# Kernel tuning notes

Hardware: AMD Instinct MI355X
Metric: run time of the kernel (lower is better)

Reference implementation:

```python
import jax, jax.numpy as jnp
import numpy as np

B, N1, N2, D = 4096, 16, 32, 30   # node batch, 1st-hop nbrs, 2nd-hop nbrs, nodeDataLen
H, HD = 6, 5                       # heads, head_dim (embed_dim = size_out*heads = 30)
LH = 64                            # linear_hidden
NEG_SLOPE = 0.02


def setup_inputs() -> dict:
    key = jax.random.key(0)
    ks = jax.random.split(key, 20)
    def w(k, shape, std=0.2):
        return jax.random.normal(k, shape, dtype=jnp.float32) * std
    return {
        "x2": jax.random.normal(ks[0], (B, N1, N2, D), dtype=jnp.float32),
        "self_feat": jax.random.normal(ks[1], (B, D), dtype=jnp.float32),
        # second-hop GraphLayer params (size_in=30 -> embed 30)
        "lin_w2": w(ks[2], (D, D)), "lin_b2": jnp.zeros((D,), jnp.float32),
        "in_w2": w(ks[3], (3 * D, D), 0.1), "in_b2": jnp.zeros((3 * D,), jnp.float32),
        "out_w2": w(ks[4], (D, D), 0.1), "out_b2": jnp.zeros((D,), jnp.float32),
        # first-hop GraphLayer params
        "lin_w1": w(ks[5], (D, D)), "lin_b1": jnp.zeros((D,), jnp.float32),
        "in_w1": w(ks[6], (3 * D, D), 0.1), "in_b1": jnp.zeros((3 * D,), jnp.float32),
        "out_w1": w(ks[7], (D, D), 0.1), "out_b1": jnp.zeros((D,), jnp.float32),
        # classification MLP
        "cw1": w(ks[8], (LH, D), 0.02), "cb1": jnp.zeros((LH,), jnp.float32),
        "cw2": w(ks[9], (LH, LH), 0.02), "cb2": jnp.zeros((LH,), jnp.float32),
        "cw3": w(ks[10], (2, LH), 0.02), "cb3": jnp.zeros((2,), jnp.float32),
    }


def graph_layer(x, lw, lb, iw, ib, ow, ob):
    """x: [S, D] -> Linear + LeakyReLU(0.02) + MHA(self) + mean over S -> [D].
    Dropout(0.2) is identity in eval mode."""
    S = x.shape[0]
    y = jax.nn.leaky_relu(x @ lw.T + lb, NEG_SLOPE)          # [S, D]
    qkv = y @ iw.T + ib                                       # [S, 3D] packed in_proj
    q, k, v = jnp.split(qkv, 3, axis=-1)
    q = q.reshape(S, H, HD)
    k = k.reshape(S, H, HD)
    v = v.reshape(S, H, HD)
    scores = jnp.einsum('shd,thd->hst', q, k) / np.float32(np.sqrt(HD))
    att = jax.nn.softmax(scores, axis=-1)                     # [H, S, S]
    o = jnp.einsum('hst,thd->shd', att, v).reshape(S, H * HD) # [S, D]
    o = o @ ow.T + ob
    return o.mean(axis=0)                                     # [D]


def reference(x2, self_feat,
              lin_w2, lin_b2, in_w2, in_b2, out_w2, out_b2,
              lin_w1, lin_b1, in_w1, in_b1, out_w1, out_b1,
              cw1, cb1, cw2, cb2, cw3, cb3):
    gl2 = lambda x: graph_layer(x, lin_w2, lin_b2, in_w2, in_b2, out_w2, out_b2)
    h1 = jax.vmap(jax.vmap(gl2))(x2)                          # [B, N1, D] second-hop aggregation
    seq = jnp.concatenate([h1, self_feat[:, None, :]], axis=1)  # [B, N1+1, D] append current node
    gl1 = lambda x: graph_layer(x, lin_w1, lin_b1, in_w1, in_b1, out_w1, out_b1)
    emb = jax.vmap(gl1)(seq)                                  # [B, D]
    h = jax.nn.leaky_relu(emb @ cw1.T + cb1, NEG_SLOPE)
    h = jax.nn.leaky_relu(h @ cw2.T + cb2, NEG_SLOPE)
    logits = h @ cw3.T + cb3                                  # [B, 2]
    # original applies Softmax(dim=0) to the 1-D 2-vector per node == softmax over classes
    return jax.nn.softmax(logits, axis=-1)
```

## Files before the change

kernel.cpp:

```cpp
#include <hip/hip_runtime.h>
#include <math.h>

#define LRELU(v) fmaxf((v), 0.02f * (v))

typedef __attribute__((ext_vector_type(8)))  short short8;
typedef __attribute__((ext_vector_type(4)))  float f32x4;
typedef __attribute__((ext_vector_type(16))) float f32x16;
typedef __attribute__((ext_vector_type(2)))  int   int2v;
typedef __attribute__((ext_vector_type(4)))  int   int4v;

__device__ inline short f2bf(float f) {
    unsigned u = __builtin_bit_cast(unsigned, f);
    unsigned r = (u + 0x7FFFu + ((u >> 16) & 1u)) >> 16;
    return (short)r;
}
__device__ inline int cvt_pk_bf16(float lo, float hi) {
    int r;
    asm("v_cvt_pk_bf16_f32 %0, %1, %2" : "=v"(r) : "v"(lo), "v"(hi));
    return r;
}
__device__ inline float exp2_asm(float x) {
    float r;
    asm("v_exp_f32 %0, %1" : "=v"(r) : "v"(x));
    return r;
}

#define RS5L  0.6451994329f

__global__ __launch_bounds__(256, 4) void fused_kernel(
    const float* __restrict__ x2, const float* __restrict__ self_feat,
    const float* __restrict__ lw2, const float* __restrict__ lb2,
    const float* __restrict__ iw2, const float* __restrict__ ib2,
    const float* __restrict__ ow2, const float* __restrict__ ob2,
    const float* __restrict__ lw1, const float* __restrict__ lb1,
    const float* __restrict__ iw1, const float* __restrict__ ib1,
    const float* __restrict__ ow1, const float* __restrict__ ob1,
    const float* __restrict__ cw1, const float* __restrict__ cb1,
    const float* __restrict__ cw2, const float* __restrict__ cb2,
    const float* __restrict__ cw3, const float* __restrict__ cb3,
    float* __restrict__ out)
{
    __shared__ __attribute__((aligned(16))) short y_lds[2][32][40];
    __shared__ __attribute__((aligned(16))) short qmf[2][6][33][8];
    __shared__ __attribute__((aligned(16))) short kmf[2][6][33][8];
    __shared__ __attribute__((aligned(16))) short vbf[2][6][8][40];
    __shared__ __attribute__((aligned(16))) float h1fp[2][16][33];
    __shared__ float obar1[32];
    __shared__ float embb[32];
    __shared__ float hb1[64];
    __shared__ float hb2[64];
    __shared__ float lg[2];

    const int tid  = threadIdx.x;
    const int lane = tid & 63;
    const int w    = tid >> 6;
    const int l15  = lane & 15;
    const int lq   = lane >> 4;
    const int h5   = lane >> 5;
    const int scol = lane & 31;
    const int rowz = (lane < 32) ? scol : 32;

    for (int i = tid; i < 1584; i += 256) { ((int*)qmf)[i] = 0; ((int*)kmf)[i] = 0; }
    for (int i = tid; i < 1920; i += 256) ((int*)vbf)[i] = 0;
    if (tid < 2) obar1[30 + tid] = 0.0f;

    const int di = w & 1, si = w >> 1;
    const int jtA = (3 * w) >> 1, jtB = (3 * w + 2) >> 1;
    short8 blw2f; float lbv2v;
    {
        int d = di * 16 + l15;
        #pragma unroll
        for (int i = 0; i < 8; ++i) {
            int k = lq * 8 + i;
            blw2f[i] = f2bf((d < 30 && k < 30) ? lw2[d * 30 + k] : 0.0f);
        }
        lbv2v = (d < 30) ? lb2[d] : 0.0f;
    }
    short8 biwA2, biwB2; float ibvA2, ibvB2;
    {
        int jA = jtA * 16 + l15, jB = jtB * 16 + l15;
        #pragma unroll
        for (int i = 0; i < 8; ++i) {
            int k = lq * 8 + i;
            biwA2[i] = f2bf((jA < 90 && k < 30) ? iw2[jA * 30 + k] : 0.0f);
            biwB2[i] = f2bf((jB < 90 && k < 30) ? iw2[jB * 30 + k] : 0.0f);
        }
        ibvA2 = (jA < 90) ? ib2[jA] : 0.0f;
        ibvB2 = (jB < 90) ? ib2[jB] : 0.0f;
    }
    __syncthreads();

    const long node = (long)blockIdx.x;
    const float* xbase = x2 + node * (16L * 960);
    const float* sfp   = self_feat + node * 30;
    const int dd = (scol < 30) ? scol : 0;

    for (int it = 0; it < 8; ++it) {

        {
            int s = si * 16 + l15;
            #pragma unroll
            for (int pr = 0; pr < 2; ++pr) {
                const float* xr = xbase + (2 * it + pr) * 960 + s * 30 + lq * 8;
                float xv[8];
                #pragma unroll
                for (int i = 0; i < 8; ++i) {
                    int k = lq * 8 + i;
                    xv[i] = (k < 30) ? xr[i] : 0.0f;
                }
                int4v ai;
                ai.x = cvt_pk_bf16(xv[0], xv[1]);
                ai.y = cvt_pk_bf16(xv[2], xv[3]);
                ai.z = cvt_pk_bf16(xv[4], xv[5]);
                ai.w = cvt_pk_bf16(xv[6], xv[7]);
                short8 af = __builtin_bit_cast(short8, ai);
                f32x4 c = {0.0f, 0.0f, 0.0f, 0.0f};
                c = __builtin_amdgcn_mfma_f32_16x16x32_bf16(af, blw2f, c, 0, 0, 0);
                float y0 = LRELU(c[0] + lbv2v), y1 = LRELU(c[1] + lbv2v);
                float y2 = LRELU(c[2] + lbv2v), y3 = LRELU(c[3] + lbv2v);
                int p01 = cvt_pk_bf16(y0, y1), p23 = cvt_pk_bf16(y2, y3);
                int row = si * 16 + lq * 4, col = di * 16 + l15;
                y_lds[pr][row + 0][col] = (short)p01;
                y_lds[pr][row + 1][col] = (short)(p01 >> 16);
                y_lds[pr][row + 2][col] = (short)p23;
                y_lds[pr][row + 3][col] = (short)(p23 >> 16);
            }
        }
        __syncthreads();

        {
            #pragma unroll
            for (int pr = 0; pr < 2; ++pr) {
                short8 a0 = *(const short8*)&y_lds[pr][l15][lq * 8];
                short8 a1 = *(const short8*)&y_lds[pr][16 + l15][lq * 8];
                #pragma unroll
                for (int t = 0; t < 3; ++t) {
                    int T = 3 * w + t, jt = T >> 1, si_ = T & 1;
                    short8 a = si_ ? a1 : a0;
                    short8 b = (jt == jtA) ? biwA2 : biwB2;
                    float ibv = (jt == jtA) ? ibvA2 : ibvB2;
                    f32x4 c = {0.0f, 0.0f, 0.0f, 0.0f};
                    c = __builtin_amdgcn_mfma_f32_16x16x32_bf16(a, b, c, 0, 0, 0);
                    int j = jt * 16 + l15;
                    int s0 = si_ * 16 + lq * 4;
                    if (j < 30) {
                        int h = j / 5, e = j - 5 * h;
                        int p01 = cvt_pk_bf16(c[0] + ibv, c[1] + ibv);
                        int p23 = cvt_pk_bf16(c[2] + ibv, c[3] + ibv);
                        qmf[pr][h][s0 + 0][e] = (short)p01;
                        qmf[pr][h][s0 + 1][e] = (short)(p01 >> 16);
                        qmf[pr][h][s0 + 2][e] = (short)p23;
                        qmf[pr][h][s0 + 3][e] = (short)(p23 >> 16);
                    } else if (j < 60) {
                        int jj = j - 30; int h = jj / 5, e = jj - 5 * h;
                        float ibl = ibv * RS5L;
                        int p01 = cvt_pk_bf16(fmaf(c[0], RS5L, ibl), fmaf(c[1], RS5L, ibl));
                        int p23 = cvt_pk_bf16(fmaf(c[2], RS5L, ibl), fmaf(c[3], RS5L, ibl));
                        kmf[pr][h][s0 + 0][e] = (short)p01;
                        kmf[pr][h][s0 + 1][e] = (short)(p01 >> 16);
                        kmf[pr][h][s0 + 2][e] = (short)p23;
                        kmf[pr][h][s0 + 3][e] = (short)(p23 >> 16);
                    } else if (j < 90) {
                        int jj = j - 60; int h = jj / 5, e = jj - 5 * h;
                        int k0 = ((s0 >> 1) & 4) | ((s0 << 1) & 8) | (s0 & 16);
                        int2v wv;
                        wv.x = cvt_pk_bf16(c[0] + ibv, c[1] + ibv);
                        wv.y = cvt_pk_bf16(c[2] + ibv, c[3] + ibv);
                        *(int2v*)&vbf[pr][h][e][k0] = wv;
                    }
                }
            }
        }
        __syncthreads();

        {
            const int pr  = w >> 1;
            const int grp = w & 1;
            float smv0, smv1, smv2;
            #pragma unroll
            for (int hh = 0; hh < 3; ++hh) {
                const int h = 3 * grp + hh;
                short8 af = *(const short8*)&kmf[pr][h][rowz][0];
                short8 bf = *(const short8*)&qmf[pr][h][rowz][0];
                f32x16 c;
                #pragma unroll
                for (int r = 0; r < 16; ++r) c[r] = 0.0f;
                c = __builtin_amdgcn_mfma_f32_32x32x16_bf16(af, bf, c, 0, 0, 0);
                float m = c[0];
                #pragma unroll
                for (int r = 1; r < 16; ++r) m = fmaxf(m, c[r]);
                m = fmaxf(m, __shfl_xor(m, 32));
                float Z = 0.0f;
                #pragma unroll
                for (int r = 0; r < 16; ++r) { c[r] = exp2_asm(c[r] - m); Z += c[r]; }
                Z += __shfl_xor(Z, 32);
                float rZ = __builtin_amdgcn_rcpf(Z) * (1.0f / 32.0f);
                int4v a1i, a2i;
                a1i.x = cvt_pk_bf16(c[0] * rZ,  c[1] * rZ);
                a1i.y = cvt_pk_bf16(c[2] * rZ,  c[3] * rZ);
                a1i.z = cvt_pk_bf16(c[4] * rZ,  c[5] * rZ);
                a1i.w = cvt_pk_bf16(c[6] * rZ,  c[7] * rZ);
                a2i.x = cvt_pk_bf16(c[8] * rZ,  c[9] * rZ);
                a2i.y = cvt_pk_bf16(c[10] * rZ, c[11] * rZ);
                a2i.z = cvt_pk_bf16(c[12] * rZ, c[13] * rZ);
                a2i.w = cvt_pk_bf16(c[14] * rZ, c[15] * rZ);
                short8 b1 = *(const short8*)&vbf[pr][h][scol & 7][8 * h5];
                short8 b2 = *(const short8*)&vbf[pr][h][scol & 7][16 + 8 * h5];
                f32x16 P;
                #pragma unroll
                for (int r = 0; r < 16; ++r) P[r] = 0.0f;
                P = __builtin_amdgcn_mfma_f32_32x32x16_bf16(
                        __builtin_bit_cast(short8, a1i), b1, P, 0, 0, 0);
                P = __builtin_amdgcn_mfma_f32_32x32x16_bf16(
                        __builtin_bit_cast(short8, a2i), b2, P, 0, 0, 0);
                float sm = 0.0f;
                #pragma unroll
                for (int r = 0; r < 16; ++r) sm += P[r];
                sm += __shfl_xor(sm, 32);
                if (hh == 0) smv0 = sm; else if (hh == 1) smv1 = sm; else smv2 = sm;
            }
            float part = 0.0f;
            #pragma unroll
            for (int hh = 0; hh < 3; ++hh) {
                float smv = (hh == 0) ? smv0 : (hh == 1) ? smv1 : smv2;
                #pragma unroll
                for (int e = 0; e < 5; ++e) {
                    float ov = __shfl(smv, e);
                    part = fmaf(ov, ow2[dd * 30 + grp * 15 + hh * 5 + e], part);
                }
            }
            if (lane < 30) h1fp[grp][2 * it + pr][lane] = part;
        }
    }
    __syncthreads();

    short8 blw1f; float lbv1v;
    {
        int d = di * 16 + l15;
        #pragma unroll
        for (int i = 0; i < 8; ++i) {
            int k = lq * 8 + i;
            blw1f[i] = f2bf((d < 30 && k < 30) ? lw1[d * 30 + k] : 0.0f);
        }
        lbv1v = (d < 30) ? lb1[d] : 0.0f;
    }
    short8 biwA1, biwB1; float ibvA1, ibvB1;
    {
        int jA = jtA * 16 + l15, jB = jtB * 16 + l15;
        #pragma unroll
        for (int i = 0; i < 8; ++i) {
            int k = lq * 8 + i;
            biwA1[i] = f2bf((jA < 90 && k < 30) ? iw1[jA * 30 + k] : 0.0f);
            biwB1[i] = f2bf((jB < 90 && k < 30) ? iw1[jB * 30 + k] : 0.0f);
        }
        ibvA1 = (jA < 90) ? ib1[jA] : 0.0f;
        ibvB1 = (jB < 90) ? ib1[jB] : 0.0f;
    }

    {
        float xv[8];
        if (si == 0) {
            #pragma unroll
            for (int i = 0; i < 8; ++i) {
                int k = lq * 8 + i;
                xv[i] = (k < 30)
                    ? (h1fp[0][l15][k] + h1fp[1][l15][k] + ob2[k]) : 0.0f;
            }
        } else {
            #pragma unroll
            for (int i = 0; i < 8; ++i) {
                int k = lq * 8 + i;
                xv[i] = (l15 == 0 && k < 30) ? sfp[k] : 0.0f;
            }
        }
        int4v ai;
        ai.x = cvt_pk_bf16(xv[0], xv[1]);
        ai.y = cvt_pk_bf16(xv[2], xv[3]);
        ai.z = cvt_pk_bf16(xv[4], xv[5]);
        ai.w = cvt_pk_bf16(xv[6], xv[7]);
        short8 af = __builtin_bit_cast(short8, ai);
        f32x4 c = {0.0f, 0.0f, 0.0f, 0.0f};
        c = __builtin_amdgcn_mfma_f32_16x16x32_bf16(af, blw1f, c, 0, 0, 0);
        float y0 = LRELU(c[0] + lbv1v), y1 = LRELU(c[1] + lbv1v);
        float y2 = LRELU(c[2] + lbv1v), y3 = LRELU(c[3] + lbv1v);
        int p01 = cvt_pk_bf16(y0, y1), p23 = cvt_pk_bf16(y2, y3);
        int row = si * 16 + lq * 4, col = di * 16 + l15;
        y_lds[0][row + 0][col] = (short)p01;
        y_lds[0][row + 1][col] = (short)(p01 >> 16);
        y_lds[0][row + 2][col] = (short)p23;
        y_lds[0][row + 3][col] = (short)(p23 >> 16);
    }
    __syncthreads();

    {
        short8 a0 = *(const short8*)&y_lds[0][l15][lq * 8];
        short8 a1 = *(const short8*)&y_lds[0][16 + l15][lq * 8];
        #pragma unroll
        for (int t = 0; t < 3; ++t) {
            int T = 3 * w + t, jt = T >> 1, si_ = T & 1;
            short8 a = si_ ? a1 : a0;
            short8 b = (jt == jtA) ? biwA1 : biwB1;
            float ibv = (jt == jtA) ? ibvA1 : ibvB1;
            f32x4 c = {0.0f, 0.0f, 0.0f, 0.0f};
            c = __builtin_amdgcn_mfma_f32_16x16x32_bf16(a, b, c, 0, 0, 0);
            int j = jt * 16 + l15;
            int s0 = si_ * 16 + lq * 4;
            if (j < 30) {
                int h = j / 5, e = j - 5 * h;
                int p01 = cvt_pk_bf16(c[0] + ibv, c[1] + ibv);
                int p23 = cvt_pk_bf16(c[2] + ibv, c[3] + ibv);
                qmf[0][h][s0 + 0][e] = (short)p01;
                qmf[0][h][s0 + 1][e] = (short)(p01 >> 16);
                qmf[0][h][s0 + 2][e] = (short)p23;
                qmf[0][h][s0 + 3][e] = (short)(p23 >> 16);
            } else if (j < 60) {
                int jj = j - 30; int h = jj / 5, e = jj - 5 * h;
                float ibl = ibv * RS5L;
                int p01 = cvt_pk_bf16(fmaf(c[0], RS5L, ibl), fmaf(c[1], RS5L, ibl));
                int p23 = cvt_pk_bf16(fmaf(c[2], RS5L, ibl), fmaf(c[3], RS5L, ibl));
                kmf[0][h][s0 + 0][e] = (short)p01;
                kmf[0][h][s0 + 1][e] = (short)(p01 >> 16);
                kmf[0][h][s0 + 2][e] = (short)p23;
                kmf[0][h][s0 + 3][e] = (short)(p23 >> 16);
            } else if (j < 90) {
                int jj = j - 60; int h = jj / 5, e = jj - 5 * h;
                int k0 = ((s0 >> 1) & 4) | ((s0 << 1) & 8) | (s0 & 16);
                int2v wv;
                wv.x = cvt_pk_bf16(c[0] + ibv, c[1] + ibv);
                wv.y = cvt_pk_bf16(c[2] + ibv, c[3] + ibv);
                *(int2v*)&vbf[0][h][e][k0] = wv;
            }
        }
    }
    __syncthreads();

    if (w < 3) {
        #pragma unroll
        for (int hh = 0; hh < 2; ++hh) {
            const int h = 2 * w + hh;
            short8 af = *(const short8*)&kmf[0][h][rowz][0];
            short8 bf = *(const short8*)&qmf[0][h][rowz][0];
            f32x16 c;
            #pragma unroll
            for (int r = 0; r < 16; ++r) c[r] = 0.0f;
            c = __builtin_amdgcn_mfma_f32_32x32x16_bf16(af, bf, c, 0, 0, 0);
            #pragma unroll
            for (int r = 0; r < 16; ++r) {
                int tr = (r & 3) + 8 * (r >> 2) + 4 * h5;
                c[r] = (tr < 17) ? c[r] : -1e30f;
            }
            float m = c[0];
            #pragma unroll
            for (int r = 1; r < 16; ++r) m = fmaxf(m, c[r]);
            m = fmaxf(m, __shfl_xor(m, 32));
            float Z = 0.0f;
            #pragma unroll
            for (int r = 0; r < 16; ++r) { c[r] = exp2_asm(c[r] - m); Z += c[r]; }
            Z += __shfl_xor(Z, 32);
            float rZ = __builtin_amdgcn_rcpf(Z) * (1.0f / 17.0f);
            int4v a1i, a2i;
            a1i.x = cvt_pk_bf16(c[0] * rZ,  c[1] * rZ);
            a1i.y = cvt_pk_bf16(c[2] * rZ,  c[3] * rZ);
            a1i.z = cvt_pk_bf16(c[4] * rZ,  c[5] * rZ);
            a1i.w = cvt_pk_bf16(c[6] * rZ,  c[7] * rZ);
            a2i.x = cvt_pk_bf16(c[8] * rZ,  c[9] * rZ);
            a2i.y = cvt_pk_bf16(c[10] * rZ, c[11] * rZ);
            a2i.z = cvt_pk_bf16(c[12] * rZ, c[13] * rZ);
            a2i.w = cvt_pk_bf16(c[14] * rZ, c[15] * rZ);
            short8 b1 = *(const short8*)&vbf[0][h][scol & 7][8 * h5];
            short8 b2 = *(const short8*)&vbf[0][h][scol & 7][16 + 8 * h5];
            f32x16 P;
            #pragma unroll
            for (int r = 0; r < 16; ++r) P[r] = 0.0f;
            P = __builtin_amdgcn_mfma_f32_32x32x16_bf16(
                    __builtin_bit_cast(short8, a1i), b1, P, 0, 0, 0);
            P = __builtin_amdgcn_mfma_f32_32x32x16_bf16(
                    __builtin_bit_cast(short8, a2i), b2, P, 0, 0, 0);
            float sm = 0.0f;
            #pragma unroll
            for (int r = 0; r < 8; ++r) sm += P[r];
            sm += (h5 == 0) ? P[8] : 0.0f;
            sm += __shfl_xor(sm, 32);
            if (lane < 5) obar1[h * 5 + lane] = sm;
        }
    }
    __syncthreads();

    if (tid < 240) {
        const int d = tid >> 3, jq = tid & 7;
        f32x4 ov = *(const f32x4*)&obar1[jq * 4];
        float part = 0.0f;
        #pragma unroll
        for (int i = 0; i < 4; ++i) {
            int j = jq * 4 + i;
            if (j < 30) part = fmaf(ov[i], ow1[d * 30 + j], part);
        }
        part += __shfl_down(part, 4, 8);
        part += __shfl_down(part, 2, 8);
        part += __shfl_down(part, 1, 8);
        if (jq == 0) embb[d] = part + ob1[d];
    }
    __syncthreads();

    {
        const int o = tid >> 2, kq = tid & 3;
        float part = 0.0f;
        #pragma unroll
        for (int i = 0; i < 8; ++i) {
            int k = kq * 8 + i;
            if (k < 30) part = fmaf(embb[k], cw1[o * 30 + k], part);
        }
        part += __shfl_down(part, 2, 4);
        part += __shfl_down(part, 1, 4);
        if (kq == 0) hb1[o] = LRELU(part + cb1[o]);
    }
    __syncthreads();
    {
        const int o = tid >> 2, kq = tid & 3;
        float part = 0.0f;
        #pragma unroll
        for (int i = 0; i < 16; ++i) {
            int k = kq * 16 + i;
            part = fmaf(hb1[k], cw2[o * 64 + k], part);
        }
        part += __shfl_down(part, 2, 4);
        part += __shfl_down(part, 1, 4);
        if (kq == 0) hb2[o] = LRELU(part + cb2[o]);
    }
    __syncthreads();
    if (tid < 128) {
        const int c = tid >> 6, k = tid & 63;
        float part = hb2[k] * cw3[c * 64 + k];
        part += __shfl_down(part, 32);
        part += __shfl_down(part, 16);
        part += __shfl_down(part, 8);
        part += __shfl_down(part, 4);
        part += __shfl_down(part, 2);
        part += __shfl_down(part, 1);
        if (k == 0) lg[c] = part + cb3[c];
    }
    __syncthreads();
    if (tid < 2) {
        float m = fmaxf(lg[0], lg[1]);
        float e0 = __expf(lg[0] - m), e1 = __expf(lg[1] - m);
        float pr = ((tid == 0) ? e0 : e1) / (e0 + e1);
        out[node * 2 + tid] = pr;
    }
}

extern "C" void kernel_launch(void* const* d_in, const int* in_sizes, int n_in,
                              void* d_out, int out_size, void* d_ws, size_t ws_size,
                              hipStream_t stream)
{
    const float* x2        = (const float*)d_in[0];
    const float* self_feat = (const float*)d_in[1];
    const float* lin_w2 = (const float*)d_in[2];
    const float* lin_b2 = (const float*)d_in[3];
    const float* in_w2  = (const float*)d_in[4];
    const float* in_b2  = (const float*)d_in[5];
    const float* out_w2 = (const float*)d_in[6];
    const float* out_b2 = (const float*)d_in[7];
    const float* lin_w1 = (const float*)d_in[8];
    const float* lin_b1 = (const float*)d_in[9];
    const float* in_w1  = (const float*)d_in[10];
    const float* in_b1  = (const float*)d_in[11];
    const float* out_w1 = (const float*)d_in[12];
    const float* out_b1 = (const float*)d_in[13];
    const float* cw1 = (const float*)d_in[14];
    const float* cb1 = (const float*)d_in[15];
    const float* cw2 = (const float*)d_in[16];
    const float* cb2 = (const float*)d_in[17];
    const float* cw3 = (const float*)d_in[18];
    const float* cb3 = (const float*)d_in[19];
    float* outp = (float*)d_out;

    fused_kernel<<<4096, 256, 0, stream>>>(
        x2, self_feat,
        lin_w2, lin_b2, in_w2, in_b2, out_w2, out_b2,
        lin_w1, lin_b1, in_w1, in_b1, out_w1, out_b1,
        cw1, cb1, cw2, cb2, cw3, cb3, outp);
}
```

Before: 497.6 us.

## Process one neighbor per iteration with register prefetch of next x tile

Changes the second-hop loop from two neighbors per iteration (8 iterations) to one neighbor per iteration (16 iterations), halving the LDS buffers. The global loads for the next neighbor are issued into registers before the current neighbor's MFMA work, overlapping memory latency with compute. Attention heads are redistributed across all four waves (2,2,1,1), and partial outputs are kept per wave and summed at the end. Each step now does less work per barrier and has uneven work across waves, but the smaller LDS footprint may allow higher occupancy.

```diff
diff --git a/kernel.cpp b/kernel.cpp
--- a/kernel.cpp
+++ b/kernel.cpp
@@ -40,11 +40,11 @@
     const float* __restrict__ cw3, const float* __restrict__ cb3,
     float* __restrict__ out)
 {
-    __shared__ __attribute__((aligned(16))) short y_lds[2][32][40];
-    __shared__ __attribute__((aligned(16))) short qmf[2][6][33][8];
-    __shared__ __attribute__((aligned(16))) short kmf[2][6][33][8];
-    __shared__ __attribute__((aligned(16))) short vbf[2][6][8][40];
-    __shared__ __attribute__((aligned(16))) float h1fp[2][16][33];
+    __shared__ __attribute__((aligned(16))) short y_lds[32][40];
+    __shared__ __attribute__((aligned(16))) short qmf[6][33][8];
+    __shared__ __attribute__((aligned(16))) short kmf[6][33][8];
+    __shared__ __attribute__((aligned(16))) short vbf[6][8][40];
+    __shared__ __attribute__((aligned(16))) float h1fp[4][16][33];
     __shared__ float obar1[32];
     __shared__ float embb[32];
     __shared__ float hb1[64];
@@ -60,8 +60,8 @@
     const int scol = lane & 31;
     const int rowz = (lane < 32) ? scol : 32;
 
-    for (int i = tid; i < 1584; i += 256) { ((int*)qmf)[i] = 0; ((int*)kmf)[i] = 0; }
-    for (int i = tid; i < 1920; i += 256) ((int*)vbf)[i] = 0;
+    for (int i = tid; i < 792; i += 256) { ((int*)qmf)[i] = 0; ((int*)kmf)[i] = 0; }
+    for (int i = tid; i < 960; i += 256) ((int*)vbf)[i] = 0;
     if (tid < 2) obar1[30 + tid] = 0.0f;
 
     const int di = w & 1, si = w >> 1;
@@ -94,94 +94,100 @@
     const float* xbase = x2 + node * (16L * 960);
     const float* sfp   = self_feat + node * 30;
     const int dd = (scol < 30) ? scol : 0;
-
-    for (int it = 0; it < 8; ++it) {
+    const int srow = si * 16 + l15;
+
+    float xcur[8];
+    {
+        const float* xr = xbase + srow * 30 + lq * 8;
+        #pragma unroll
+        for (int i = 0; i < 8; ++i) {
+            int k = lq * 8 + i;
+            xcur[i] = (k < 30) ? xr[i] : 0.0f;
+        }
+    }
+
+    for (int it = 0; it < 16; ++it) {
+        float xnext[8];
 
         {
-            int s = si * 16 + l15;
-            #pragma unroll
-            for (int pr = 0; pr < 2; ++pr) {
-                const float* xr = xbase + (2 * it + pr) * 960 + s * 30 + lq * 8;
-                float xv[8];
-                #pragma unroll
-                for (int i = 0; i < 8; ++i) {
-                    int k = lq * 8 + i;
-                    xv[i] = (k < 30) ? xr[i] : 0.0f;
+            int4v ai;
+            ai.x = cvt_pk_bf16(xcur[0], xcur[1]);
+            ai.y = cvt_pk_bf16(xcur[2], xcur[3]);
+            ai.z = cvt_pk_bf16(xcur[4], xcur[5]);
+            ai.w = cvt_pk_bf16(xcur[6], xcur[7]);
+            const int itn = (it < 15) ? it + 1 : it;
+            const float* xr = xbase + itn * 960 + srow * 30 + lq * 8;
+            #pragma unroll
+            for (int i = 0; i < 8; ++i) {
+                int k = lq * 8 + i;
+                xnext[i] = (k < 30) ? xr[i] : 0.0f;
+            }
+            short8 af = __builtin_bit_cast(short8, ai);
+            f32x4 c = {0.0f, 0.0f, 0.0f, 0.0f};
+            c = __builtin_amdgcn_mfma_f32_16x16x32_bf16(af, blw2f, c, 0, 0, 0);
+            float y0 = LRELU(c[0] + lbv2v), y1 = LRELU(c[1] + lbv2v);
+            float y2 = LRELU(c[2] + lbv2v), y3 = LRELU(c[3] + lbv2v);
+            int p01 = cvt_pk_bf16(y0, y1), p23 = cvt_pk_bf16(y2, y3);
+            int row = si * 16 + lq * 4, col = di * 16 + l15;
+            y_lds[row + 0][col] = (short)p01;
+            y_lds[row + 1][col] = (short)(p01 >> 16);
+            y_lds[row + 2][col] = (short)p23;
+            y_lds[row + 3][col] = (short)(p23 >> 16);
+        }
+        __syncthreads();
+
+        {
+            short8 a0 = *(const short8*)&y_lds[l15][lq * 8];
+            short8 a1 = *(const short8*)&y_lds[16 + l15][lq * 8];
+            #pragma unroll
+            for (int t = 0; t < 3; ++t) {
+                int T = 3 * w + t, jt = T >> 1, si_ = T & 1;
+                short8 a = si_ ? a1 : a0;
+                short8 b = (jt == jtA) ? biwA2 : biwB2;
+                float ibv = (jt == jtA) ? ibvA2 : ibvB2;
+                f32x4 c = {0.0f, 0.0f, 0.0f, 0.0f};
+                c = __builtin_amdgcn_mfma_f32_16x16x32_bf16(a, b, c, 0, 0, 0);
+                int j = jt * 16 + l15;
+                int s0 = si_ * 16 + lq * 4;
+                if (j < 30) {
+                    int h = j / 5, e = j - 5 * h;
+                    int p01 = cvt_pk_bf16(c[0] + ibv, c[1] + ibv);
+                    int p23 = cvt_pk_bf16(c[2] + ibv, c[3] + ibv);
+                    qmf[h][s0 + 0][e] = (short)p01;
+                    qmf[h][s0 + 1][e] = (short)(p01 >> 16);
+                    qmf[h][s0 + 2][e] = (short)p23;
+                    qmf[h][s0 + 3][e] = (short)(p23 >> 16);
+                } else if (j < 60) {
+                    int jj = j - 30; int h = jj / 5, e = jj - 5 * h;
+                    float ibl = ibv * RS5L;
+                    int p01 = cvt_pk_bf16(fmaf(c[0], RS5L, ibl), fmaf(c[1], RS5L, ibl));
+                    int p23 = cvt_pk_bf16(fmaf(c[2], RS5L, ibl), fmaf(c[3], RS5L, ibl));
+                    kmf[h][s0 + 0][e] = (short)p01;
+                    kmf[h][s0 + 1][e] = (short)(p01 >> 16);
+                    kmf[h][s0 + 2][e] = (short)p23;
+                    kmf[h][s0 + 3][e] = (short)(p23 >> 16);
+                } else if (j < 90) {
+                    int jj = j - 60; int h = jj / 5, e = jj - 5 * h;
+                    int k0 = ((s0 >> 1) & 4) | ((s0 << 1) & 8) | (s0 & 16);
+                    int2v wv;
+                    wv.x = cvt_pk_bf16(c[0] + ibv, c[1] + ibv);
+                    wv.y = cvt_pk_bf16(c[2] + ibv, c[3] + ibv);
+                    *(int2v*)&vbf[h][e][k0] = wv;
                 }
-                int4v ai;
-                ai.x = cvt_pk_bf16(xv[0], xv[1]);
-                ai.y = cvt_pk_bf16(xv[2], xv[3]);
-                ai.z = cvt_pk_bf16(xv[4], xv[5]);
-                ai.w = cvt_pk_bf16(xv[6], xv[7]);
-                short8 af = __builtin_bit_cast(short8, ai);
-                f32x4 c = {0.0f, 0.0f, 0.0f, 0.0f};
-                c = __builtin_amdgcn_mfma_f32_16x16x32_bf16(af, blw2f, c, 0, 0, 0);
-                float y0 = LRELU(c[0] + lbv2v), y1 = LRELU(c[1] + lbv2v);
-                float y2 = LRELU(c[2] + lbv2v), y3 = LRELU(c[3] + lbv2v);
-                int p01 = cvt_pk_bf16(y0, y1), p23 = cvt_pk_bf16(y2, y3);
-                int row = si * 16 + lq * 4, col = di * 16 + l15;
-                y_lds[pr][row + 0][col] = (short)p01;
-                y_lds[pr][row + 1][col] = (short)(p01 >> 16);
-                y_lds[pr][row + 2][col] = (short)p23;
-                y_lds[pr][row + 3][col] = (short)(p23 >> 16);
             }
         }
         __syncthreads();
 
         {
-            #pragma unroll
-            for (int pr = 0; pr < 2; ++pr) {
-                short8 a0 = *(const short8*)&y_lds[pr][l15][lq * 8];
-                short8 a1 = *(const short8*)&y_lds[pr][16 + l15][lq * 8];
-                #pragma unroll
-                for (int t = 0; t < 3; ++t) {
-                    int T = 3 * w + t, jt = T >> 1, si_ = T & 1;
-                    short8 a = si_ ? a1 : a0;
-                    short8 b = (jt == jtA) ? biwA2 : biwB2;
-                    float ibv = (jt == jtA) ? ibvA2 : ibvB2;
-                    f32x4 c = {0.0f, 0.0f, 0.0f, 0.0f};
-                    c = __builtin_amdgcn_mfma_f32_16x16x32_bf16(a, b, c, 0, 0, 0);
-                    int j = jt * 16 + l15;
-                    int s0 = si_ * 16 + lq * 4;
-                    if (j < 30) {
-                        int h = j / 5, e = j - 5 * h;
-                        int p01 = cvt_pk_bf16(c[0] + ibv, c[1] + ibv);
-                        int p23 = cvt_pk_bf16(c[2] + ibv, c[3] + ibv);
-                        qmf[pr][h][s0 + 0][e] = (short)p01;
-                        qmf[pr][h][s0 + 1][e] = (short)(p01 >> 16);
-                        qmf[pr][h][s0 + 2][e] = (short)p23;
-                        qmf[pr][h][s0 + 3][e] = (short)(p23 >> 16);
-                    } else if (j < 60) {
-                        int jj = j - 30; int h = jj / 5, e = jj - 5 * h;
-                        float ibl = ibv * RS5L;
-                        int p01 = cvt_pk_bf16(fmaf(c[0], RS5L, ibl), fmaf(c[1], RS5L, ibl));
-                        int p23 = cvt_pk_bf16(fmaf(c[2], RS5L, ibl), fmaf(c[3], RS5L, ibl));
-                        kmf[pr][h][s0 + 0][e] = (short)p01;
-                        kmf[pr][h][s0 + 1][e] = (short)(p01 >> 16);
-                        kmf[pr][h][s0 + 2][e] = (short)p23;
-                        kmf[pr][h][s0 + 3][e] = (short)(p23 >> 16);
-                    } else if (j < 90) {
-                        int jj = j - 60; int h = jj / 5, e = jj - 5 * h;
-                        int k0 = ((s0 >> 1) & 4) | ((s0 << 1) & 8) | (s0 & 16);
-                        int2v wv;
-                        wv.x = cvt_pk_bf16(c[0] + ibv, c[1] + ibv);
-                        wv.y = cvt_pk_bf16(c[2] + ibv, c[3] + ibv);
-                        *(int2v*)&vbf[pr][h][e][k0] = wv;
-                    }
-                }
-            }
-        }
-        __syncthreads();
-
-        {
-            const int pr  = w >> 1;
-            const int grp = w & 1;
-            float smv0, smv1, smv2;
-            #pragma unroll
-            for (int hh = 0; hh < 3; ++hh) {
-                const int h = 3 * grp + hh;
-                short8 af = *(const short8*)&kmf[pr][h][rowz][0];
-                short8 bf = *(const short8*)&qmf[pr][h][rowz][0];
+            const int hbase = (w < 2) ? (2 * w) : (2 + w);
+            const bool two = (w < 2);
+            float smv0 = 0.0f, smv1 = 0.0f;
+            #pragma unroll
+            for (int hh = 0; hh < 2; ++hh) {
+                if (hh == 1 && !two) continue;
+                const int h = hbase + hh;
+                short8 af = *(const short8*)&kmf[h][rowz][0];
+                short8 bf = *(const short8*)&qmf[h][rowz][0];
                 f32x16 c;
                 #pragma unroll
                 for (int r = 0; r < 16; ++r) c[r] = 0.0f;
@@ -204,8 +210,8 @@
                 a2i.y = cvt_pk_bf16(c[10] * rZ, c[11] * rZ);
                 a2i.z = cvt_pk_bf16(c[12] * rZ, c[13] * rZ);
                 a2i.w = cvt_pk_bf16(c[14] * rZ, c[15] * rZ);
-                short8 b1 = *(const short8*)&vbf[pr][h][scol & 7][8 * h5];
-                short8 b2 = *(const short8*)&vbf[pr][h][scol & 7][16 + 8 * h5];
+                short8 b1 = *(const short8*)&vbf[h][scol & 7][8 * h5];
+                short8 b2 = *(const short8*)&vbf[h][scol & 7][16 + 8 * h5];
                 f32x16 P;
                 #pragma unroll
                 for (int r = 0; r < 16; ++r) P[r] = 0.0f;
@@ -217,20 +223,25 @@
                 #pragma unroll
                 for (int r = 0; r < 16; ++r) sm += P[r];
                 sm += __shfl_xor(sm, 32);
-                if (hh == 0) smv0 = sm; else if (hh == 1) smv1 = sm; else smv2 = sm;
+                if (hh == 0) smv0 = sm; else smv1 = sm;
             }
             float part = 0.0f;
             #pragma unroll
-            for (int hh = 0; hh < 3; ++hh) {
-                float smv = (hh == 0) ? smv0 : (hh == 1) ? smv1 : smv2;
+            for (int e = 0; e < 5; ++e) {
+                float ov = __shfl(smv0, e);
+                part = fmaf(ov, ow2[dd * 30 + hbase * 5 + e], part);
+            }
+            if (two) {
                 #pragma unroll
                 for (int e = 0; e < 5; ++e) {
-                    float ov = __shfl(smv, e);
-                    part = fmaf(ov, ow2[dd * 30 + grp * 15 + hh * 5 + e], part);
+                    float ov = __shfl(smv1, e);
+                    part = fmaf(ov, ow2[dd * 30 + (hbase + 1) * 5 + e], part);
                 }
             }
-            if (lane < 30) h1fp[grp][2 * it + pr][lane] = part;
-        }
+            if (lane < 30) h1fp[w][it][lane] = part;
+        }
+        #pragma unroll
+        for (int i = 0; i < 8; ++i) xcur[i] = xnext[i];
     }
     __syncthreads();
 
@@ -264,7 +275,8 @@
             for (int i = 0; i < 8; ++i) {
                 int k = lq * 8 + i;
                 xv[i] = (k < 30)
-                    ? (h1fp[0][l15][k] + h1fp[1][l15][k] + ob2[k]) : 0.0f;
+                    ? (h1fp[0][l15][k] + h1fp[1][l15][k]
+                       + h1fp[2][l15][k] + h1fp[3][l15][k] + ob2[k]) : 0.0f;
             }
         } else {
             #pragma unroll
@@ -285,16 +297,16 @@
         float y2 = LRELU(c[2] + lbv1v), y3 = LRELU(c[3] + lbv1v);
         int p01 = cvt_pk_bf16(y0, y1), p23 = cvt_pk_bf16(y2, y3);
         int row = si * 16 + lq * 4, col = di * 16 + l15;
-        y_lds[0][row + 0][col] = (short)p01;
-        y_lds[0][row + 1][col] = (short)(p01 >> 16);
-        y_lds[0][row + 2][col] = (short)p23;
-        y_lds[0][row + 3][col] = (short)(p23 >> 16);
-    }
-    __syncthreads();
-
-    {
-        short8 a0 = *(const short8*)&y_lds[0][l15][lq * 8];
-        short8 a1 = *(const short8*)&y_lds[0][16 + l15][lq * 8];
+        y_lds[row + 0][col] = (short)p01;
+        y_lds[row + 1][col] = (short)(p01 >> 16);
+        y_lds[row + 2][col] = (short)p23;
+        y_lds[row + 3][col] = (short)(p23 >> 16);
+    }
+    __syncthreads();
+
+    {
+        short8 a0 = *(const short8*)&y_lds[l15][lq * 8];
+        short8 a1 = *(const short8*)&y_lds[16 + l15][lq * 8];
         #pragma unroll
         for (int t = 0; t < 3; ++t) {
             int T = 3 * w + t, jt = T >> 1, si_ = T & 1;
@@ -309,26 +321,26 @@
                 int h = j / 5, e = j - 5 * h;
                 int p01 = cvt_pk_bf16(c[0] + ibv, c[1] + ibv);
                 int p23 = cvt_pk_bf16(c[2] + ibv, c[3] + ibv);
-                qmf[0][h][s0 + 0][e] = (short)p01;
-                qmf[0][h][s0 + 1][e] = (short)(p01 >> 16);
-                qmf[0][h][s0 + 2][e] = (short)p23;
-                qmf[0][h][s0 + 3][e] = (short)(p23 >> 16);
+                qmf[h][s0 + 0][e] = (short)p01;
+                qmf[h][s0 + 1][e] = (short)(p01 >> 16);
+                qmf[h][s0 + 2][e] = (short)p23;
+                qmf[h][s0 + 3][e] = (short)(p23 >> 16);
             } else if (j < 60) {
                 int jj = j - 30; int h = jj / 5, e = jj - 5 * h;
                 float ibl = ibv * RS5L;
                 int p01 = cvt_pk_bf16(fmaf(c[0], RS5L, ibl), fmaf(c[1], RS5L, ibl));
                 int p23 = cvt_pk_bf16(fmaf(c[2], RS5L, ibl), fmaf(c[3], RS5L, ibl));
-                kmf[0][h][s0 + 0][e] = (short)p01;
-                kmf[0][h][s0 + 1][e] = (short)(p01 >> 16);
-                kmf[0][h][s0 + 2][e] = (short)p23;
-                kmf[0][h][s0 + 3][e] = (short)(p23 >> 16);
+                kmf[h][s0 + 0][e] = (short)p01;
+                kmf[h][s0 + 1][e] = (short)(p01 >> 16);
+                kmf[h][s0 + 2][e] = (short)p23;
+                kmf[h][s0 + 3][e] = (short)(p23 >> 16);
             } else if (j < 90) {
                 int jj = j - 60; int h = jj / 5, e = jj - 5 * h;
                 int k0 = ((s0 >> 1) & 4) | ((s0 << 1) & 8) | (s0 & 16);
                 int2v wv;
                 wv.x = cvt_pk_bf16(c[0] + ibv, c[1] + ibv);
                 wv.y = cvt_pk_bf16(c[2] + ibv, c[3] + ibv);
-                *(int2v*)&vbf[0][h][e][k0] = wv;
+                *(int2v*)&vbf[h][e][k0] = wv;
             }
         }
     }
@@ -338,8 +350,8 @@
         #pragma unroll
         for (int hh = 0; hh < 2; ++hh) {
             const int h = 2 * w + hh;
-            short8 af = *(const short8*)&kmf[0][h][rowz][0];
-            short8 bf = *(const short8*)&qmf[0][h][rowz][0];
+            short8 af = *(const short8*)&kmf[h][rowz][0];
+            short8 bf = *(const short8*)&qmf[h][rowz][0];
             f32x16 c;
             #pragma unroll
             for (int r = 0; r < 16; ++r) c[r] = 0.0f;
@@ -367,8 +379,8 @@
             a2i.y = cvt_pk_bf16(c[10] * rZ, c[11] * rZ);
             a2i.z = cvt_pk_bf16(c[12] * rZ, c[13] * rZ);
             a2i.w = cvt_pk_bf16(c[14] * rZ, c[15] * rZ);
-            short8 b1 = *(const short8*)&vbf[0][h][scol & 7][8 * h5];
-            short8 b2 = *(const short8*)&vbf[0][h][scol & 7][16 + 8 * h5];
+            short8 b1 = *(const short8*)&vbf[h][scol & 7][8 * h5];
+            short8 b2 = *(const short8*)&vbf[h][scol & 7][16 + 8 * h5];
             f32x16 P;
             #pragma unroll
             for (int r = 0; r < 16; ++r) P[r] = 0.0f;
```

Result: slower. 530.4 us (+6.6%).
